# Kernel tuning notes

Measured on AMD Instinct MI355X. Metric: run time of the kernel, lower is better.

Reference implementation:

```python
import jax, jax.numpy as jnp
import numpy as np

# Dimensions (see shape_source)
B, N, F = 2, 400, 246          # batch, nodes, node features
S = 1                           # edge feature channels
C = 32                          # stack_channels
LBL = 1440                      # shape_node_labels
STACK_IN = 2 * F + 2 * S        # concat([x_i, x_j, e_ij, e_ji])
NODE_IN = F + 2 * C             # concat([x, agg_in, agg_out])


def _glorot(key, shape):
    fan_in, fan_out = shape[0], shape[1]
    lim = np.sqrt(6.0 / (fan_in + fan_out)).astype(np.float32)
    return jax.random.uniform(key, shape, jnp.float32, -lim, lim)


def setup_inputs() -> dict:
    key = jax.random.key(0)
    ks = jax.random.split(key, 12)
    x = jax.random.normal(ks[0], (B, N, F), jnp.float32)
    a = (jax.random.uniform(ks[1], (B, N, N)) < 0.10).astype(jnp.float32)
    e = jax.random.uniform(ks[2], (B, N, N, S), jnp.float32)
    return {
        "x": x,
        "a": a,
        "e": e,
        # XENetConv stack model: single Dense(C) + PReLU (per-channel alpha)
        "W_stack": _glorot(ks[3], (STACK_IN, C)),
        "b_stack": jnp.zeros((C,), jnp.float32),
        "alpha": jnp.full((C,), 0.25, jnp.float32),
        # attention heads: Dense(1, sigmoid) each
        "W_att_i": _glorot(ks[4], (C, 1)),
        "b_att_i": jnp.zeros((1,), jnp.float32),
        "W_att_j": _glorot(ks[5], (C, 1)),
        "b_att_j": jnp.zeros((1,), jnp.float32),
        # node model: Dense(F) over concat([x, agg_in, agg_out]) (linear)
        "W_node": _glorot(ks[6], (NODE_IN, F)),
        "b_node": jnp.zeros((F,), jnp.float32),
        # trailing Dense(shape_node_labels, linear)
        "W_out": _glorot(ks[7], (F, LBL)),
        "b_out": jnp.zeros((LBL,), jnp.float32),
    }


def reference(x, a, e, W_stack, b_stack, alpha, W_att_i, b_att_i,
              W_att_j, b_att_j, W_node, b_node, W_out, b_out):
    # --- XENetConvBatch ---
    # pairwise stack: [x_i, x_j, e_ij, e_ji] over all (i, j) node pairs
    x_i = jnp.broadcast_to(x[:, :, None, :], (B, N, N, F))
    x_j = jnp.broadcast_to(x[:, None, :, :], (B, N, N, F))
    e_t = jnp.transpose(e, (0, 2, 1, 3))                     # e_ji
    stack = jnp.concatenate([x_i, x_j, e, e_t], axis=-1)     # (B,N,N,2F+2S)
    s = jnp.einsum("bijk,kc->bijc", stack, W_stack) + b_stack  # (B,N,N,C)
    s = jnp.where(s >= 0, s, alpha * s)                      # PReLU
    s = s * a[..., None]                                     # mask non-edges
    # attention (sigmoid gates for incoming / outgoing aggregation)
    att_i = jax.nn.sigmoid(s @ W_att_i + b_att_i)            # (B,N,N,1)
    att_j = jax.nn.sigmoid(s @ W_att_j + b_att_j)
    agg_i = jnp.sum(s * att_i, axis=2)                       # (B,N,C) sum over j
    agg_j = jnp.sum(s * att_j, axis=1)                       # (B,N,C) sum over i
    x_new = jnp.concatenate([x, agg_i, agg_j], axis=-1) @ W_node + b_node  # (B,N,F)
    # Net discards the edge output of the conv; final linear Dense
    out = x_new @ W_out + b_out                              # (B,N,LBL)
    return out
```

## Files before the change

kernel.cpp:

```cpp
#include <hip/hip_runtime.h>
#include <math.h>

#define B_ 2
#define N_ 400
#define F_ 246
#define C_ 32
#define LBL_ 1440
#define NODE_IN_ 310

#define KX_ 320
#define KN_ 256

#define T_ABUF (800 * KX_)
#define T_W2T  (64 * KX_)
#define T_WNT  (256 * KX_)
#define T_WOT  (LBL_ * KN_)

typedef __attribute__((ext_vector_type(8))) short bf16x8;
typedef __attribute__((ext_vector_type(4))) float f32x4;

__device__ __forceinline__ short f2bf(float f) {
    unsigned u = __float_as_uint(f);
    return (short)((u + 0x7FFF + ((u >> 16) & 1)) >> 16);
}

__global__ void k_prep(const float* __restrict__ x, const float* __restrict__ Ws,
                       const float* __restrict__ Wn, const float* __restrict__ Wo,
                       short* __restrict__ Abuf, short* __restrict__ W2T,
                       short* __restrict__ WnT, short* __restrict__ WoT) {
    __shared__ short tile[32][33];
    int bx = blockIdx.x, tid = threadIdx.x;
    if (bx < 800) {
        if (tid < F_) Abuf[bx * KX_ + tid] = f2bf(x[bx * F_ + tid]);
        return;
    }
    bx -= 800;
    int tx = tid & 31, ty = tid >> 5;
    if (bx < 360) {
        int n0 = (bx % 45) * 32, k0 = (bx / 45) * 32;
        #pragma unroll
        for (int r = 0; r < 4; ++r) {
            int k = k0 + ty + r * 8;
            tile[ty + r * 8][tx] = (k < F_) ? f2bf(Wo[k * LBL_ + n0 + tx]) : (short)0;
        }
        __syncthreads();
        #pragma unroll
        for (int r = 0; r < 4; ++r)
            WoT[(size_t)(n0 + ty + r * 8) * KN_ + k0 + tx] = tile[tx][ty + r * 8];
        return;
    }
    bx -= 360;
    if (bx < 80) {
        int n0 = (bx % 8) * 32, k0 = (bx / 8) * 32;
        #pragma unroll
        for (int r = 0; r < 4; ++r) {
            int k = k0 + ty + r * 8, n = n0 + tx;
            tile[ty + r * 8][tx] =
                (n < F_ && k < NODE_IN_) ? f2bf(Wn[k * F_ + n]) : (short)0;
        }
        __syncthreads();
        #pragma unroll
        for (int r = 0; r < 4; ++r)
            WnT[(size_t)(n0 + ty + r * 8) * KX_ + k0 + tx] = tile[tx][ty + r * 8];
        return;
    }
    bx -= 80;
    {
        int t = bx * 256 + tid;
        if (t < 64 * KX_) {
            int n = t / KX_, k = t - n * KX_;
            float v = 0.f;
            if (k < F_) v = (n < C_) ? Ws[k * C_ + n] : Ws[(F_ + k) * C_ + (n - C_)];
            W2T[t] = f2bf(v);
        }
    }
}

template <int K>
__device__ __forceinline__ f32x4 mfma_tile(const short* __restrict__ A,
                                           const short* __restrict__ BT,
                                           int m0, int n0, int lane) {
    int r = lane & 15, quad = lane >> 4;
    const short* ap = A + (size_t)(m0 + r) * K + quad * 8;
    const short* bp = BT + (size_t)(n0 + r) * K + quad * 8;
    f32x4 acc = {0.f, 0.f, 0.f, 0.f};
    #pragma unroll
    for (int kk = 0; kk < K; kk += 32) {
        bf16x8 av = *(const bf16x8*)(ap + kk);
        bf16x8 bv = *(const bf16x8*)(bp + kk);
        acc = __builtin_amdgcn_mfma_f32_16x16x32_bf16(av, bv, acc, 0, 0, 0);
    }
    return acc;
}

template <int K>
__device__ __forceinline__ void mfma_tile2(const short* __restrict__ A,
                                           const short* __restrict__ BT,
                                           int m0, int n0, int lane,
                                           f32x4& acc0, f32x4& acc1) {
    int r = lane & 15, quad = lane >> 4;
    const short* ap = A + (size_t)(m0 + r) * K + quad * 8;
    const short* b0 = BT + (size_t)(n0 + r) * K + quad * 8;
    const short* b1 = BT + (size_t)(n0 + 16 + r) * K + quad * 8;
    #pragma unroll
    for (int kk = 0; kk < K; kk += 32) {
        bf16x8 av  = *(const bf16x8*)(ap + kk);
        bf16x8 bv0 = *(const bf16x8*)(b0 + kk);
        bf16x8 bv1 = *(const bf16x8*)(b1 + kk);
        acc0 = __builtin_amdgcn_mfma_f32_16x16x32_bf16(av, bv0, acc0, 0, 0, 0);
        acc1 = __builtin_amdgcn_mfma_f32_16x16x32_bf16(av, bv1, acc1, 0, 0, 0);
    }
}

__global__ void k_pq(const short* __restrict__ Abuf, const short* __restrict__ W2T,
                     float* __restrict__ PQ) {
    int lane = threadIdx.x;
    int m0 = blockIdx.x * 16, n0 = blockIdx.y * 16;
    f32x4 acc = mfma_tile<KX_>(Abuf, W2T, m0, n0, lane);
    int n = n0 + (lane & 15), mb = m0 + (lane >> 4) * 4;
    #pragma unroll
    for (int r = 0; r < 4; ++r)
        PQ[(size_t)(mb + r) * 64 + n] = acc[r];
}

__global__ void k_agg(const float* __restrict__ a, const float* __restrict__ e,
                      const float* __restrict__ Ws, const float* __restrict__ bs,
                      const float* __restrict__ alpha,
                      const float* __restrict__ Wai, const float* __restrict__ bai,
                      const float* __restrict__ Waj, const float* __restrict__ baj,
                      const float* __restrict__ PQ, short* __restrict__ Abuf) {
    int blk  = blockIdx.x;
    int mode = (blk >= B_ * N_) ? 1 : 0;
    int row  = mode ? blk - B_ * N_ : blk;
    int b = row / N_, n = row % N_;
    int tid = threadIdx.x;
    int c = tid & 31, g = tid >> 5;

    float w3  = Ws[(2 * F_) * C_ + c];
    float w4  = Ws[(2 * F_ + 1) * C_ + c];
    float bsc = bs[c];
    float alc = alpha[c];
    float wat = mode ? Waj[c] : Wai[c];
    float bat = mode ? baj[0] : bai[0];

    float ownc = PQ[(size_t)row * 64 + (mode ? 32 : 0) + c];
    const float* oth = PQ + (size_t)b * N_ * 64 + (mode ? 0 : 32) + c;
    const float* abase = a + (size_t)b * N_ * N_;
    const float* ebase = e + (size_t)b * N_ * N_;

    float acc = 0.f;
    #pragma unroll 4
    for (int m = g; m < N_; m += 8) {
        float aij  = mode ? abase[m * N_ + n] : abase[n * N_ + m];
        float er   = ebase[n * N_ + m];
        float ec   = ebase[m * N_ + n];
        float othv = oth[(size_t)m * 64];
        if (aij != 0.f) {
            float eij = mode ? ec : er;
            float eji = mode ? er : ec;
            float raw = ownc + othv + eij * w3 + eji * w4 + bsc;
            float s = (raw >= 0.f ? raw : alc * raw) * aij;
            float t2 = s * wat;
            t2 += __shfl_xor(t2, 1, 32);
            t2 += __shfl_xor(t2, 2, 32);
            t2 += __shfl_xor(t2, 4, 32);
            t2 += __shfl_xor(t2, 8, 32);
            t2 += __shfl_xor(t2, 16, 32);
            float att = 1.f / (1.f + __expf(-(t2 + bat)));
            acc += s * att;
        }
    }
    __shared__ float part[8][C_ + 1];
    part[g][c] = acc;
    __syncthreads();
    if (tid < C_) {
        float tot = 0.f;
        #pragma unroll
        for (int gg = 0; gg < 8; ++gg) tot += part[gg][tid];
        Abuf[(size_t)row * KX_ + F_ + mode * C_ + tid] = f2bf(tot);
    }
}

__global__ void k_node(const short* __restrict__ Abuf, const short* __restrict__ WnT,
                       const float* __restrict__ bn, short* __restrict__ XN16) {
    int lane = threadIdx.x;
    int m0 = blockIdx.x * 16, n0 = blockIdx.y * 32;
    f32x4 a0 = {0,0,0,0}, a1 = {0,0,0,0};
    mfma_tile2<KX_>(Abuf, WnT, m0, n0, lane, a0, a1);
    int col = lane & 15, mb = m0 + (lane >> 4) * 4;
    #pragma unroll
    for (int h = 0; h < 2; ++h) {
        int nn = n0 + h * 16 + col;
        f32x4 acc = h ? a1 : a0;
        float bv = (nn < F_) ? bn[nn] : 0.f;
        #pragma unroll
        for (int r = 0; r < 4; ++r)
            XN16[(size_t)(mb + r) * KN_ + nn] =
                (nn < F_) ? f2bf(acc[r] + bv) : (short)0;
    }
}

__global__ void k_out(const short* __restrict__ XN16, const short* __restrict__ WoT,
                      const float* __restrict__ bo, float* __restrict__ out) {
    int lane = threadIdx.x;
    int m0 = blockIdx.x * 16, n0 = blockIdx.y * 32;
    f32x4 a0 = {0,0,0,0}, a1 = {0,0,0,0};
    mfma_tile2<KN_>(XN16, WoT, m0, n0, lane, a0, a1);
    int col = lane & 15, mb = m0 + (lane >> 4) * 4;
    #pragma unroll
    for (int h = 0; h < 2; ++h) {
        int nn = n0 + h * 16 + col;
        f32x4 acc = h ? a1 : a0;
        float bv = bo[nn];
        #pragma unroll
        for (int r = 0; r < 4; ++r)
            out[(size_t)(mb + r) * LBL_ + nn] = acc[r] + bv;
    }
}

extern "C" void kernel_launch(void* const* d_in, const int* in_sizes, int n_in,
                              void* d_out, int out_size, void* d_ws, size_t ws_size,
                              hipStream_t stream) {
    const float* x   = (const float*)d_in[0];
    const float* a   = (const float*)d_in[1];
    const float* e   = (const float*)d_in[2];
    const float* Ws  = (const float*)d_in[3];
    const float* bs  = (const float*)d_in[4];
    const float* al  = (const float*)d_in[5];
    const float* Wai = (const float*)d_in[6];
    const float* bai = (const float*)d_in[7];
    const float* Waj = (const float*)d_in[8];
    const float* baj = (const float*)d_in[9];
    const float* Wn  = (const float*)d_in[10];
    const float* bn  = (const float*)d_in[11];
    const float* Wo  = (const float*)d_in[12];
    const float* bo  = (const float*)d_in[13];

    float* PQ   = (float*)d_ws;
    short* Abuf = (short*)(PQ + 800 * 64);
    short* W2T  = Abuf + T_ABUF;
    short* WnT  = W2T + T_W2T;
    short* WoT  = WnT + T_WNT;
    short* XN16 = WoT + T_WOT;

    k_prep<<<1320, 256, 0, stream>>>(x, Ws, Wn, Wo, Abuf, W2T, WnT, WoT);
    k_pq  <<<dim3(50, 4),  64, 0, stream>>>(Abuf, W2T, PQ);
    k_agg <<<2 * B_ * N_, 256, 0, stream>>>(a, e, Ws, bs, al, Wai, bai, Waj, baj,
                                            PQ, Abuf);
    k_node<<<dim3(50, 8),  64, 0, stream>>>(Abuf, WnT, bn, XN16);
    k_out <<<dim3(50, 45), 64, 0, stream>>>(XN16, WoT, bo, (float*)d_out);
}
```

Before: 126.7 us.

## Fuse PQ projection into prep kernel and node+output GEMMs into one kernel

The PQ projection is now computed inside the prep kernel straight from fp32 x and Ws, which removes the W2T staging buffer and one launch. The node GEMM and the output GEMM are merged into a single 1024-thread kernel that keeps the bf16 node features in shared memory, so the XN16 global round trip and another launch go away. Launches drop from five to three. The cost is that the node GEMM is recomputed in each of the 5 y-blocks per row tile, and the PQ path converts fp32 to bf16 with uncoalesced per-lane loads.

```diff
diff --git a/kernel.cpp b/kernel.cpp
--- a/kernel.cpp
+++ b/kernel.cpp
@@ -12,7 +12,6 @@
 #define KN_ 256
 
 #define T_ABUF (800 * KX_)
-#define T_W2T  (64 * KX_)
 #define T_WNT  (256 * KX_)
 #define T_WOT  (LBL_ * KN_)
 
@@ -22,58 +21,6 @@
 __device__ __forceinline__ short f2bf(float f) {
     unsigned u = __float_as_uint(f);
     return (short)((u + 0x7FFF + ((u >> 16) & 1)) >> 16);
-}
-
-__global__ void k_prep(const float* __restrict__ x, const float* __restrict__ Ws,
-                       const float* __restrict__ Wn, const float* __restrict__ Wo,
-                       short* __restrict__ Abuf, short* __restrict__ W2T,
-                       short* __restrict__ WnT, short* __restrict__ WoT) {
-    __shared__ short tile[32][33];
-    int bx = blockIdx.x, tid = threadIdx.x;
-    if (bx < 800) {
-        if (tid < F_) Abuf[bx * KX_ + tid] = f2bf(x[bx * F_ + tid]);
-        return;
-    }
-    bx -= 800;
-    int tx = tid & 31, ty = tid >> 5;
-    if (bx < 360) {
-        int n0 = (bx % 45) * 32, k0 = (bx / 45) * 32;
-        #pragma unroll
-        for (int r = 0; r < 4; ++r) {
-            int k = k0 + ty + r * 8;
-            tile[ty + r * 8][tx] = (k < F_) ? f2bf(Wo[k * LBL_ + n0 + tx]) : (short)0;
-        }
-        __syncthreads();
-        #pragma unroll
-        for (int r = 0; r < 4; ++r)
-            WoT[(size_t)(n0 + ty + r * 8) * KN_ + k0 + tx] = tile[tx][ty + r * 8];
-        return;
-    }
-    bx -= 360;
-    if (bx < 80) {
-        int n0 = (bx % 8) * 32, k0 = (bx / 8) * 32;
-        #pragma unroll
-        for (int r = 0; r < 4; ++r) {
-            int k = k0 + ty + r * 8, n = n0 + tx;
-            tile[ty + r * 8][tx] =
-                (n < F_ && k < NODE_IN_) ? f2bf(Wn[k * F_ + n]) : (short)0;
-        }
-        __syncthreads();
-        #pragma unroll
-        for (int r = 0; r < 4; ++r)
-            WnT[(size_t)(n0 + ty + r * 8) * KX_ + k0 + tx] = tile[tx][ty + r * 8];
-        return;
-    }
-    bx -= 80;
-    {
-        int t = bx * 256 + tid;
-        if (t < 64 * KX_) {
-            int n = t / KX_, k = t - n * KX_;
-            float v = 0.f;
-            if (k < F_) v = (n < C_) ? Ws[k * C_ + n] : Ws[(F_ + k) * C_ + (n - C_)];
-            W2T[t] = f2bf(v);
-        }
-    }
 }
 
 template <int K>
@@ -93,34 +40,77 @@
     return acc;
 }
 
-template <int K>
-__device__ __forceinline__ void mfma_tile2(const short* __restrict__ A,
-                                           const short* __restrict__ BT,
-                                           int m0, int n0, int lane,
-                                           f32x4& acc0, f32x4& acc1) {
-    int r = lane & 15, quad = lane >> 4;
-    const short* ap = A + (size_t)(m0 + r) * K + quad * 8;
-    const short* b0 = BT + (size_t)(n0 + r) * K + quad * 8;
-    const short* b1 = BT + (size_t)(n0 + 16 + r) * K + quad * 8;
-    #pragma unroll
-    for (int kk = 0; kk < K; kk += 32) {
-        bf16x8 av  = *(const bf16x8*)(ap + kk);
-        bf16x8 bv0 = *(const bf16x8*)(b0 + kk);
-        bf16x8 bv1 = *(const bf16x8*)(b1 + kk);
-        acc0 = __builtin_amdgcn_mfma_f32_16x16x32_bf16(av, bv0, acc0, 0, 0, 0);
-        acc1 = __builtin_amdgcn_mfma_f32_16x16x32_bf16(av, bv1, acc1, 0, 0, 0);
-    }
-}
-
-__global__ void k_pq(const short* __restrict__ Abuf, const short* __restrict__ W2T,
-                     float* __restrict__ PQ) {
-    int lane = threadIdx.x;
-    int m0 = blockIdx.x * 16, n0 = blockIdx.y * 16;
-    f32x4 acc = mfma_tile<KX_>(Abuf, W2T, m0, n0, lane);
-    int n = n0 + (lane & 15), mb = m0 + (lane >> 4) * 4;
-    #pragma unroll
-    for (int r = 0; r < 4; ++r)
-        PQ[(size_t)(mb + r) * 64 + n] = acc[r];
+__global__ void k_pre(const float* __restrict__ x, const float* __restrict__ Ws,
+                      const float* __restrict__ Wn, const float* __restrict__ Wo,
+                      float* __restrict__ PQ, short* __restrict__ Abuf,
+                      short* __restrict__ WnT, short* __restrict__ WoT) {
+    __shared__ short tile[32][33];
+    int bx = blockIdx.x, tid = threadIdx.x;
+    if (bx < 50) {
+        int w = tid >> 6, lane = tid & 63;
+        int m0 = bx * 16, n = w * 16 + (lane & 15);
+        int r = lane & 15, quad = lane >> 4;
+        const float* xrow = x + (size_t)(m0 + r) * F_;
+        f32x4 acc = {0.f, 0.f, 0.f, 0.f};
+        #pragma unroll
+        for (int kk = 0; kk < 256; kk += 32) {
+            int kb = kk + quad * 8;
+            bf16x8 av, bv;
+            #pragma unroll
+            for (int j = 0; j < 8; ++j) {
+                int k = kb + j;
+                av[j] = (k < F_) ? f2bf(xrow[k]) : (short)0;
+                float f = 0.f;
+                if (k < F_) f = (n < C_) ? Ws[k * C_ + n]
+                                         : Ws[(F_ + k) * C_ + (n - C_)];
+                bv[j] = f2bf(f);
+            }
+            acc = __builtin_amdgcn_mfma_f32_16x16x32_bf16(av, bv, acc, 0, 0, 0);
+        }
+        int mb = m0 + quad * 4;
+        #pragma unroll
+        for (int rr = 0; rr < 4; ++rr)
+            PQ[(size_t)(mb + rr) * 64 + n] = acc[rr];
+        return;
+    }
+    bx -= 50;
+    if (bx < 100) {
+        int r0 = bx * 8;
+        for (int idx = tid; idx < 8 * F_; idx += 256) {
+            int lr = idx / F_, k = idx - lr * F_;
+            Abuf[(size_t)(r0 + lr) * KX_ + k] = f2bf(x[(size_t)(r0 + lr) * F_ + k]);
+        }
+        return;
+    }
+    bx -= 100;
+    int tx = tid & 31, ty = tid >> 5;
+    if (bx < 360) {
+        int n0 = (bx % 45) * 32, k0 = (bx / 45) * 32;
+        #pragma unroll
+        for (int r = 0; r < 4; ++r) {
+            int k = k0 + ty + r * 8;
+            tile[ty + r * 8][tx] = (k < F_) ? f2bf(Wo[k * LBL_ + n0 + tx]) : (short)0;
+        }
+        __syncthreads();
+        #pragma unroll
+        for (int r = 0; r < 4; ++r)
+            WoT[(size_t)(n0 + ty + r * 8) * KN_ + k0 + tx] = tile[tx][ty + r * 8];
+        return;
+    }
+    bx -= 360;
+    {
+        int n0 = (bx % 8) * 32, k0 = (bx / 8) * 32;
+        #pragma unroll
+        for (int r = 0; r < 4; ++r) {
+            int k = k0 + ty + r * 8, n = n0 + tx;
+            tile[ty + r * 8][tx] =
+                (n < F_ && k < NODE_IN_) ? f2bf(Wn[k * F_ + n]) : (short)0;
+        }
+        __syncthreads();
+        #pragma unroll
+        for (int r = 0; r < 4; ++r)
+            WnT[(size_t)(n0 + ty + r * 8) * KX_ + k0 + tx] = tile[tx][ty + r * 8];
+    }
 }
 
 __global__ void k_agg(const float* __restrict__ a, const float* __restrict__ e,
@@ -181,40 +171,45 @@
     }
 }
 
-__global__ void k_node(const short* __restrict__ Abuf, const short* __restrict__ WnT,
-                       const float* __restrict__ bn, short* __restrict__ XN16) {
-    int lane = threadIdx.x;
-    int m0 = blockIdx.x * 16, n0 = blockIdx.y * 32;
-    f32x4 a0 = {0,0,0,0}, a1 = {0,0,0,0};
-    mfma_tile2<KX_>(Abuf, WnT, m0, n0, lane, a0, a1);
-    int col = lane & 15, mb = m0 + (lane >> 4) * 4;
-    #pragma unroll
-    for (int h = 0; h < 2; ++h) {
-        int nn = n0 + h * 16 + col;
-        f32x4 acc = h ? a1 : a0;
+__global__ __launch_bounds__(1024, 1)
+void k_nodeout(const short* __restrict__ Abuf, const short* __restrict__ WnT,
+               const float* __restrict__ bn, const short* __restrict__ WoT,
+               const float* __restrict__ bo, float* __restrict__ out) {
+    __shared__ short Xs[16][264];
+    int tid = threadIdx.x;
+    int w = tid >> 6, lane = tid & 63;
+    int m0 = blockIdx.x * 16;
+    int col = lane & 15, quad = lane >> 4;
+
+    {
+        int n0 = w * 16;
+        f32x4 acc = mfma_tile<KX_>(Abuf, WnT, m0, n0, lane);
+        int nn = n0 + col;
         float bv = (nn < F_) ? bn[nn] : 0.f;
         #pragma unroll
         for (int r = 0; r < 4; ++r)
-            XN16[(size_t)(mb + r) * KN_ + nn] =
-                (nn < F_) ? f2bf(acc[r] + bv) : (short)0;
-    }
-}
-
-__global__ void k_out(const short* __restrict__ XN16, const short* __restrict__ WoT,
-                      const float* __restrict__ bo, float* __restrict__ out) {
-    int lane = threadIdx.x;
-    int m0 = blockIdx.x * 16, n0 = blockIdx.y * 32;
-    f32x4 a0 = {0,0,0,0}, a1 = {0,0,0,0};
-    mfma_tile2<KN_>(XN16, WoT, m0, n0, lane, a0, a1);
-    int col = lane & 15, mb = m0 + (lane >> 4) * 4;
-    #pragma unroll
-    for (int h = 0; h < 2; ++h) {
-        int nn = n0 + h * 16 + col;
-        f32x4 acc = h ? a1 : a0;
+            Xs[quad * 4 + r][nn] = (nn < F_) ? f2bf(acc[r] + bv) : (short)0;
+    }
+    __syncthreads();
+
+    const short* xbase = &Xs[0][0];
+    for (int tt = w; tt < 18; tt += 16) {
+        int n0 = (blockIdx.y * 18 + tt) * 16;
+        int r = lane & 15;
+        const short* ap = xbase + r * 264 + quad * 8;
+        const short* bp = WoT + (size_t)(n0 + r) * KN_ + quad * 8;
+        f32x4 acc = {0.f, 0.f, 0.f, 0.f};
+        #pragma unroll
+        for (int kk = 0; kk < KN_; kk += 32) {
+            bf16x8 av = *(const bf16x8*)(ap + kk);
+            bf16x8 bv = *(const bf16x8*)(bp + kk);
+            acc = __builtin_amdgcn_mfma_f32_16x16x32_bf16(av, bv, acc, 0, 0, 0);
+        }
+        int nn = n0 + col;
         float bv = bo[nn];
         #pragma unroll
-        for (int r = 0; r < 4; ++r)
-            out[(size_t)(mb + r) * LBL_ + nn] = acc[r] + bv;
+        for (int rr = 0; rr < 4; ++rr)
+            out[(size_t)(m0 + quad * 4 + rr) * LBL_ + nn] = acc[rr] + bv;
     }
 }
 
@@ -238,15 +233,12 @@
 
     float* PQ   = (float*)d_ws;
     short* Abuf = (short*)(PQ + 800 * 64);
-    short* W2T  = Abuf + T_ABUF;
-    short* WnT  = W2T + T_W2T;
+    short* WnT  = Abuf + T_ABUF;
     short* WoT  = WnT + T_WNT;
-    short* XN16 = WoT + T_WOT;
-
-    k_prep<<<1320, 256, 0, stream>>>(x, Ws, Wn, Wo, Abuf, W2T, WnT, WoT);
-    k_pq  <<<dim3(50, 4),  64, 0, stream>>>(Abuf, W2T, PQ);
-    k_agg <<<2 * B_ * N_, 256, 0, stream>>>(a, e, Ws, bs, al, Wai, bai, Waj, baj,
-                                            PQ, Abuf);
-    k_node<<<dim3(50, 8),  64, 0, stream>>>(Abuf, WnT, bn, XN16);
-    k_out <<<dim3(50, 45), 64, 0, stream>>>(XN16, WoT, bo, (float*)d_out);
-}
+
+    k_pre<<<590, 256, 0, stream>>>(x, Ws, Wn, Wo, PQ, Abuf, WnT, WoT);
+    k_agg<<<2 * B_ * N_, 256, 0, stream>>>(a, e, Ws, bs, al, Wai, bai, Waj, baj,
+                                           PQ, Abuf);
+    k_nodeout<<<dim3(50, 5), 1024, 0, stream>>>(Abuf, WnT, bn, WoT, bo,
+                                                (float*)d_out);
+}
```

Measured after the change: 132.6 us. 1.05x slower.
